# Kernel optimization log

Hardware: AMD Instinct MI355X
Metric: run time of the kernel (lower is better)

The kernel has to match this reference:

```python
import jax, jax.numpy as jnp
import numpy as np


def setup_inputs() -> dict:
    key = jax.random.key(0)
    k1, k2, k3 = jax.random.split(key, 3)
    B, H, W, D, K = 16, 32, 32, 128, 32
    x = jax.random.normal(k1, (B, H, W, D), dtype=jnp.float32)
    std = 1.0 / (K * D) ** 0.5
    codewords = jax.random.uniform(k2, (K, D), minval=-std, maxval=std, dtype=jnp.float32)
    scale = jax.random.uniform(k3, (K,), minval=-1.0, maxval=0.0, dtype=jnp.float32)
    return {"x": x, "codewords": codewords, "scale": scale}


def reference(x, codewords, scale):
    B, H, W, D = x.shape
    K = codewords.shape[0]
    X = x.reshape(B, H * W, D)                      # [B, N, D]
    # scaled squared distances: s_k * ||x_n - c_k||^2 via expansion (no BNKD tensor)
    x2 = jnp.sum(X * X, axis=-1, keepdims=True)     # [B, N, 1]
    c2 = jnp.sum(codewords * codewords, axis=-1)    # [K]
    xc = jnp.einsum('bnd,kd->bnk', X, codewords)    # [B, N, K]
    SL = scale[None, None, :] * (x2 - 2.0 * xc + c2[None, None, :])
    A = jax.nn.softmax(SL, axis=2)                  # assignment weights [B, N, K]
    # E_bk = sum_n A_bnk * (x_bn - c_k)
    E = jnp.einsum('bnk,bnd->bkd', A, X) - jnp.sum(A, axis=1)[:, :, None] * codewords[None]
    return E
```

## Files before the change

kernel.cpp:

```cpp
#include <hip/hip_runtime.h>


constexpr int NPB = 64;
constexpr int XS  = 132;

__global__ __launch_bounds__(256)
void enc_partial(const float* __restrict__ x, const float* __restrict__ cw,
                 const float* __restrict__ scale, float* __restrict__ ws)
{
    __shared__ float x_s[NPB * XS];
    __shared__ float A_s[NPB * 32];
    __shared__ float x2_s[NPB];
    __shared__ float asum_s[4 * 32];

    const int tid = threadIdx.x;
    const int b   = blockIdx.x >> 4;
    const int s   = blockIdx.x & 15;

    const float4* xg4 = (const float4*)(x + (size_t)(b * 1024 + s * NPB) * 128);
#pragma unroll
    for (int i = 0; i < 8; ++i) {
        int f = tid + 256 * i;
        float4 v = xg4[f];
        *(float4*)&x_s[(f >> 5) * XS + (f & 31) * 4] = v;
    }

    const int lane = tid & 63;
    const int k    = lane & 31;
    const int h    = lane >> 5;
    const int w    = tid >> 6;

    float4 cf[16];
    const float4* cw4 = (const float4*)(cw + k * 128 + h * 64);
    float c2 = 0.f;
#pragma unroll
    for (int i = 0; i < 16; ++i) {
        float4 c = cw4[i];
        cf[i] = c;
        c2 += c.x * c.x + c.y * c.y + c.z * c.z + c.w * c.w;
    }
    c2 += __shfl_xor(c2, 32);
    const float sck = scale[k];

    __syncthreads();

    {
        int p = tid >> 2, q = tid & 3;
        float ss = 0.f;
#pragma unroll
        for (int i = 0; i < 8; ++i) {
            float4 v = *(const float4*)&x_s[p * XS + q * 32 + 4 * i];
            ss += v.x * v.x + v.y * v.y + v.z * v.z + v.w * v.w;
        }
        ss += __shfl_xor(ss, 1);
        ss += __shfl_xor(ss, 2);
        if (q == 0) x2_s[p] = ss;
    }
    __syncthreads();

    float a_part = 0.f;
#pragma unroll 2
    for (int p = 0; p < 16; ++p) {
        const int n = (w << 4) + p;
        const float4* xr = (const float4*)&x_s[n * XS + h * 64];
        float xc = 0.f;
#pragma unroll
        for (int i = 0; i < 16; ++i) {
            float4 v = xr[i];
            xc += v.x * cf[i].x + v.y * cf[i].y + v.z * cf[i].z + v.w * cf[i].w;
        }
        xc += __shfl_xor(xc, 32);

        float sl = sck * (x2_s[n] - 2.f * xc + c2);
        float m = sl;
#pragma unroll
        for (int msk = 16; msk >= 1; msk >>= 1) m = fmaxf(m, __shfl_xor(m, msk));
        float e = __expf(sl - m);
        float den = e;
#pragma unroll
        for (int msk = 16; msk >= 1; msk >>= 1) den += __shfl_xor(den, msk);
        float a = e / den;
        A_s[n * 32 + k] = a;
        a_part += a;
    }
    if (h == 0) asum_s[w * 32 + k] = a_part;
    __syncthreads();

    {
        const int kg = tid >> 5;
        const int dg = tid & 31;
        float acc[4][4];
#pragma unroll
        for (int i = 0; i < 4; ++i)
#pragma unroll
            for (int j = 0; j < 4; ++j) acc[i][j] = 0.f;

#pragma unroll 8
        for (int n = 0; n < NPB; ++n) {
            float4 a4 = *(const float4*)&A_s[n * 32 + kg * 4];
            float4 x4 = *(const float4*)&x_s[n * XS + dg * 4];
            acc[0][0] += a4.x * x4.x; acc[0][1] += a4.x * x4.y;
            acc[0][2] += a4.x * x4.z; acc[0][3] += a4.x * x4.w;
            acc[1][0] += a4.y * x4.x; acc[1][1] += a4.y * x4.y;
            acc[1][2] += a4.y * x4.z; acc[1][3] += a4.y * x4.w;
            acc[2][0] += a4.z * x4.x; acc[2][1] += a4.z * x4.y;
            acc[2][2] += a4.z * x4.z; acc[2][3] += a4.z * x4.w;
            acc[3][0] += a4.w * x4.x; acc[3][1] += a4.w * x4.y;
            acc[3][2] += a4.w * x4.z; acc[3][3] += a4.w * x4.w;
        }

        float as[4];
#pragma unroll
        for (int i = 0; i < 4; ++i)
            as[i] = asum_s[kg * 4 + i] + asum_s[32 + kg * 4 + i] +
                    asum_s[64 + kg * 4 + i] + asum_s[96 + kg * 4 + i];

        float* wb = ws + (size_t)(b * 16 + s) * 4096;
#pragma unroll
        for (int i = 0; i < 4; ++i) {
            const int kk = kg * 4 + i;
            float4 c4 = *(const float4*)&cw[kk * 128 + dg * 4];
            float4 r;
            r.x = acc[i][0] - as[i] * c4.x;
            r.y = acc[i][1] - as[i] * c4.y;
            r.z = acc[i][2] - as[i] * c4.z;
            r.w = acc[i][3] - as[i] * c4.w;
            *(float4*)&wb[kk * 128 + dg * 4] = r;
        }
    }
}

__global__ __launch_bounds__(256)
void enc_reduce(const float* __restrict__ ws, float* __restrict__ out)
{
    const int gid = blockIdx.x * 256 + threadIdx.x;
    const int b   = gid >> 10;
    const int j4  = gid & 1023;
    const float4* base = (const float4*)ws + (size_t)b * 16384 + j4;
    float4 acc = {0.f, 0.f, 0.f, 0.f};
#pragma unroll
    for (int s = 0; s < 16; ++s) {
        float4 v = base[(size_t)s * 1024];
        acc.x += v.x; acc.y += v.y; acc.z += v.z; acc.w += v.w;
    }
    ((float4*)out)[gid] = acc;
}

extern "C" void kernel_launch(void* const* d_in, const int* in_sizes, int n_in,
                              void* d_out, int out_size, void* d_ws, size_t ws_size,
                              hipStream_t stream)
{
    const float* x     = (const float*)d_in[0];
    const float* cw    = (const float*)d_in[1];
    const float* scale = (const float*)d_in[2];
    float* out = (float*)d_out;
    float* ws  = (float*)d_ws;

    enc_partial<<<256, 256, 0, stream>>>(x, cw, scale, ws);
    enc_reduce<<<64, 256, 0, stream>>>(ws, out);
}
```

Measured before the change: 78.46 us.

## Halve points per block to launch more blocks, add ILP accumulators

Each block now handles 32 points instead of 64, so the partial kernel launches 512 blocks instead of 256 and fills more of the GPU's compute units. The dot-product and reduction loops use multiple independent accumulators to break serial add dependencies. In exchange the workspace doubles, and the reduce kernel must sum 32 partials per output instead of 16, which adds global memory traffic.

New measurement: 75.94 us. -3.2%, faster.

```diff
diff --git a/kernel.cpp b/kernel.cpp
--- a/kernel.cpp
+++ b/kernel.cpp
@@ -1,7 +1,7 @@
 #include <hip/hip_runtime.h>
 
 
-constexpr int NPB = 64;
+constexpr int NPB = 32;
 constexpr int XS  = 132;
 
 __global__ __launch_bounds__(256)
@@ -14,12 +14,12 @@
     __shared__ float asum_s[4 * 32];
 
     const int tid = threadIdx.x;
-    const int b   = blockIdx.x >> 4;
-    const int s   = blockIdx.x & 15;
+    const int b   = blockIdx.x >> 5;
+    const int s   = blockIdx.x & 31;
 
     const float4* xg4 = (const float4*)(x + (size_t)(b * 1024 + s * NPB) * 128);
 #pragma unroll
-    for (int i = 0; i < 8; ++i) {
+    for (int i = 0; i < 4; ++i) {
         int f = tid + 256 * i;
         float4 v = xg4[f];
         *(float4*)&x_s[(f >> 5) * XS + (f & 31) * 4] = v;
@@ -32,43 +32,50 @@
 
     float4 cf[16];
     const float4* cw4 = (const float4*)(cw + k * 128 + h * 64);
-    float c2 = 0.f;
+    float c2a = 0.f, c2b = 0.f;
 #pragma unroll
-    for (int i = 0; i < 16; ++i) {
-        float4 c = cw4[i];
-        cf[i] = c;
-        c2 += c.x * c.x + c.y * c.y + c.z * c.z + c.w * c.w;
+    for (int i = 0; i < 16; i += 2) {
+        float4 c0 = cw4[i], c1 = cw4[i + 1];
+        cf[i] = c0; cf[i + 1] = c1;
+        c2a += c0.x * c0.x + c0.y * c0.y + c0.z * c0.z + c0.w * c0.w;
+        c2b += c1.x * c1.x + c1.y * c1.y + c1.z * c1.z + c1.w * c1.w;
     }
+    float c2 = c2a + c2b;
     c2 += __shfl_xor(c2, 32);
     const float sck = scale[k];
 
     __syncthreads();
 
     {
-        int p = tid >> 2, q = tid & 3;
+        int p = tid >> 3, q = tid & 7;
         float ss = 0.f;
 #pragma unroll
-        for (int i = 0; i < 8; ++i) {
-            float4 v = *(const float4*)&x_s[p * XS + q * 32 + 4 * i];
+        for (int i = 0; i < 4; ++i) {
+            float4 v = *(const float4*)&x_s[p * XS + q * 16 + 4 * i];
             ss += v.x * v.x + v.y * v.y + v.z * v.z + v.w * v.w;
         }
         ss += __shfl_xor(ss, 1);
         ss += __shfl_xor(ss, 2);
+        ss += __shfl_xor(ss, 4);
         if (q == 0) x2_s[p] = ss;
     }
     __syncthreads();
 
     float a_part = 0.f;
-#pragma unroll 2
-    for (int p = 0; p < 16; ++p) {
-        const int n = (w << 4) + p;
+#pragma unroll
+    for (int p = 0; p < 8; ++p) {
+        const int n = (w << 3) + p;
         const float4* xr = (const float4*)&x_s[n * XS + h * 64];
-        float xc = 0.f;
+        float xc0 = 0.f, xc1 = 0.f, xc2 = 0.f, xc3 = 0.f;
 #pragma unroll
-        for (int i = 0; i < 16; ++i) {
-            float4 v = xr[i];
-            xc += v.x * cf[i].x + v.y * cf[i].y + v.z * cf[i].z + v.w * cf[i].w;
+        for (int i = 0; i < 16; i += 4) {
+            float4 v0 = xr[i + 0], v1 = xr[i + 1], v2 = xr[i + 2], v3 = xr[i + 3];
+            xc0 += v0.x * cf[i+0].x + v0.y * cf[i+0].y + v0.z * cf[i+0].z + v0.w * cf[i+0].w;
+            xc1 += v1.x * cf[i+1].x + v1.y * cf[i+1].y + v1.z * cf[i+1].z + v1.w * cf[i+1].w;
+            xc2 += v2.x * cf[i+2].x + v2.y * cf[i+2].y + v2.z * cf[i+2].z + v2.w * cf[i+2].w;
+            xc3 += v3.x * cf[i+3].x + v3.y * cf[i+3].y + v3.z * cf[i+3].z + v3.w * cf[i+3].w;
         }
+        float xc = (xc0 + xc1) + (xc2 + xc3);
         xc += __shfl_xor(xc, 32);
 
         float sl = sck * (x2_s[n] - 2.f * xc + c2);
@@ -115,7 +122,7 @@
             as[i] = asum_s[kg * 4 + i] + asum_s[32 + kg * 4 + i] +
                     asum_s[64 + kg * 4 + i] + asum_s[96 + kg * 4 + i];
 
-        float* wb = ws + (size_t)(b * 16 + s) * 4096;
+        float* wb = ws + (size_t)(b * 32 + s) * 4096;
 #pragma unroll
         for (int i = 0; i < 4; ++i) {
             const int kk = kg * 4 + i;
@@ -136,14 +143,25 @@
     const int gid = blockIdx.x * 256 + threadIdx.x;
     const int b   = gid >> 10;
     const int j4  = gid & 1023;
-    const float4* base = (const float4*)ws + (size_t)b * 16384 + j4;
-    float4 acc = {0.f, 0.f, 0.f, 0.f};
+    const float4* base = (const float4*)ws + (size_t)b * 32768 + j4;
+    float4 a0 = {0,0,0,0}, a1 = {0,0,0,0}, a2 = {0,0,0,0}, a3 = {0,0,0,0};
 #pragma unroll
-    for (int s = 0; s < 16; ++s) {
-        float4 v = base[(size_t)s * 1024];
-        acc.x += v.x; acc.y += v.y; acc.z += v.z; acc.w += v.w;
+    for (int s = 0; s < 32; s += 4) {
+        float4 v0 = base[(size_t)(s + 0) * 1024];
+        float4 v1 = base[(size_t)(s + 1) * 1024];
+        float4 v2 = base[(size_t)(s + 2) * 1024];
+        float4 v3 = base[(size_t)(s + 3) * 1024];
+        a0.x += v0.x; a0.y += v0.y; a0.z += v0.z; a0.w += v0.w;
+        a1.x += v1.x; a1.y += v1.y; a1.z += v1.z; a1.w += v1.w;
+        a2.x += v2.x; a2.y += v2.y; a2.z += v2.z; a2.w += v2.w;
+        a3.x += v3.x; a3.y += v3.y; a3.z += v3.z; a3.w += v3.w;
     }
-    ((float4*)out)[gid] = acc;
+    float4 r;
+    r.x = (a0.x + a1.x) + (a2.x + a3.x);
+    r.y = (a0.y + a1.y) + (a2.y + a3.y);
+    r.z = (a0.z + a1.z) + (a2.z + a3.z);
+    r.w = (a0.w + a1.w) + (a2.w + a3.w);
+    ((float4*)out)[gid] = r;
 }
 
 extern "C" void kernel_launch(void* const* d_in, const int* in_sizes, int n_in,
@@ -156,6 +174,6 @@
     float* out = (float*)d_out;
     float* ws  = (float*)d_ws;
 
-    enc_partial<<<256, 256, 0, stream>>>(x, cw, scale, ws);
+    enc_partial<<<512, 256, 0, stream>>>(x, cw, scale, ws);
     enc_reduce<<<64, 256, 0, stream>>>(ws, out);
 }
```
